# Kernel optimization log

Measured on AMD Instinct MI355X. Metric: run time of the kernel, lower is better.

## Reference

```python
import jax, jax.numpy as jnp
import numpy as np

D_MODEL = 64


def setup_inputs() -> dict:
    key = jax.random.key(0)
    kq, kk, kv, km = jax.random.split(key, 4)
    B, S, d = 8, 4096, D_MODEL
    Q = jax.random.normal(kq, (B, S, d), dtype=jnp.float32)
    K = jax.random.normal(kk, (B, S, d), dtype=jnp.float32)
    V = jax.random.normal(kv, (B, S, d), dtype=jnp.float32)
    mask = jax.random.uniform(km, (S, S), dtype=jnp.float32)
    return {"Q": Q, "K": K, "V": V, "mask": mask}


def reference(Q, K, V, mask):
    scale = 1.0 / np.sqrt(D_MODEL).astype(np.float32)
    # scores: [B, S, S]
    scores = jnp.einsum("bqd,bkd->bqk", Q, K) * scale
    probs = jax.nn.softmax(scores, axis=-1)
    # post-softmax multiplicative mask + renormalization over masked probs
    masked = probs * mask[None, :, :]
    masked = masked / jnp.sum(masked, axis=-1, keepdims=True)
    return jnp.einsum("bqk,bkd->bqd", masked, V)
```

## Files before the change

### kernel.cpp

```cpp
#include <hip/hip_runtime.h>
#include <hip/hip_bf16.h>

#define S_LEN 4096
#define DMODEL 64
#define QBLK 128
#define NQT (S_LEN / QBLK)
#define KBLK 32
#define NKT (S_LEN / KBLK)
#define NSPLIT 4
#define NROWS ((size_t)8 * S_LEN)
#define NELEM ((size_t)8 * S_LEN * DMODEL)
#define TSZ 2048
#define QSCALE 0.180336880f

typedef __attribute__((ext_vector_type(8))) short bf16x8;
typedef __attribute__((ext_vector_type(4))) float f32x4;
typedef __attribute__((ext_vector_type(8))) unsigned short us8;
typedef __attribute__((ext_vector_type(4))) unsigned int u32x4;

#define LDS_BARRIER()                                            \
    do {                                                         \
        asm volatile("s_waitcnt lgkmcnt(0)" ::: "memory");       \
        __builtin_amdgcn_s_barrier();                            \
    } while (0)

__device__ __forceinline__ float bf2f(unsigned short u) {
    unsigned int x = ((unsigned int)u) << 16;
    return __builtin_bit_cast(float, x);
}
__device__ __forceinline__ unsigned short f2bf(float f) {
    unsigned int u = __builtin_bit_cast(unsigned int, f);
    u += 0x7FFFu + ((u >> 16) & 1u);
    return (unsigned short)(u >> 16);
}
__device__ __forceinline__ unsigned int packbf2(float lo, float hi) {
    __hip_bfloat162 h = __float22bfloat162_rn(float2{lo, hi});
    unsigned int w;
    __builtin_memcpy(&w, &h, sizeof(w));
    return w;
}
__device__ __forceinline__ bf16x8 cvt8s(const float* __restrict__ p, float c) {
    f32x4 a = *(const f32x4*)p;
    f32x4 b = *(const f32x4*)(p + 4);
    bf16x8 r;
    r[0] = (short)f2bf(a[0] * c); r[1] = (short)f2bf(a[1] * c);
    r[2] = (short)f2bf(a[2] * c); r[3] = (short)f2bf(a[3] * c);
    r[4] = (short)f2bf(b[0] * c); r[5] = (short)f2bf(b[1] * c);
    r[6] = (short)f2bf(b[2] * c); r[7] = (short)f2bf(b[3] * c);
    return r;
}

__global__ __launch_bounds__(256)
void convert_all(const float* __restrict__ K, const float* __restrict__ V,
                 const float* __restrict__ M,
                 unsigned short* __restrict__ Ktt, unsigned short* __restrict__ Vtt,
                 unsigned short* __restrict__ Mt) {
    const int t = threadIdx.x;
    int bid = blockIdx.x;

    if (bid < 1024) {
        const int b  = bid >> 7;
        const int kt = bid & 127;
        const int l = t & 63, frag = t >> 6;
        const int j = l & 15, g = l >> 4;
        const int row = kt * KBLK + ((frag >> 1) & 1) * 16 + j;
        const int col = (frag & 1) * 32 + g * 8;
        const float* src = K + ((size_t)b * S_LEN + row) * DMODEL + col;
        f32x4 a = *(const f32x4*)src;
        f32x4 c = *(const f32x4*)(src + 4);
        us8 o;
        o[0] = f2bf(a[0]); o[1] = f2bf(a[1]); o[2] = f2bf(a[2]); o[3] = f2bf(a[3]);
        o[4] = f2bf(c[0]); o[5] = f2bf(c[1]); o[6] = f2bf(c[2]); o[7] = f2bf(c[3]);
        *(us8*)(Ktt + ((size_t)(b * NKT + kt)) * TSZ + t * 8) = o;
    } else if (bid < 2048) {
        bid -= 1024;
        __shared__ unsigned short lk[KBLK][68];
        const int b  = bid >> 7;
        const int kt = bid & 127;
        {
            const int key = t >> 3, d0 = (t & 7) * 8;
            const float* src = V + ((size_t)b * S_LEN + kt * KBLK + key) * DMODEL + d0;
            f32x4 a = *(const f32x4*)src;
            f32x4 c = *(const f32x4*)(src + 4);
            lk[key][d0 + 0] = f2bf(a[0]); lk[key][d0 + 1] = f2bf(a[1]);
            lk[key][d0 + 2] = f2bf(a[2]); lk[key][d0 + 3] = f2bf(a[3]);
            lk[key][d0 + 4] = f2bf(c[0]); lk[key][d0 + 5] = f2bf(c[1]);
            lk[key][d0 + 6] = f2bf(c[2]); lk[key][d0 + 7] = f2bf(c[3]);
        }
        __syncthreads();
        {
            const int l = t & 63, dt = t >> 6;
            const int j = l & 15, g = l >> 4;
            us8 o;
            #pragma unroll
            for (int e = 0; e < 8; ++e) {
                const int key = 16 * (e >> 2) + 4 * g + (e & 3);
                o[e] = lk[key][dt * 16 + j];
            }
            *(us8*)(Vtt + ((size_t)(b * NKT + kt)) * TSZ + t * 8) = o;
        }
    } else {
        bid -= 2048;
        const int qt  = bid >> 8;
        const int rem = bid & 255;
        const int kt  = rem >> 1;
        const int h   = rem & 1;
        const int l = t & 63, w = t >> 6;
        const int j = l & 15, g = l >> 4;
        const int row = qt * QBLK + w * 32 + h * 16 + j;
        const float* src = M + ((size_t)row) * S_LEN + kt * KBLK;
        f32x4 a = *(const f32x4*)(src + 4 * g);
        f32x4 c = *(const f32x4*)(src + 16 + 4 * g);
        us8 o;
        o[0] = f2bf(a[0]); o[1] = f2bf(a[1]); o[2] = f2bf(a[2]); o[3] = f2bf(a[3]);
        o[4] = f2bf(c[0]); o[5] = f2bf(c[1]); o[6] = f2bf(c[2]); o[7] = f2bf(c[3]);
        *(us8*)(Mt + (((size_t)(qt * NKT + kt)) * 2 + h) * TSZ + t * 8) = o;
    }
}

template <int SPLITS>
__global__ __launch_bounds__(256, 4)
void attn_frag(const float* __restrict__ Q,
               const unsigned short* __restrict__ Ktt,
               const unsigned short* __restrict__ Vtt,
               const unsigned short* __restrict__ Mt,
               float* __restrict__ Pacc, float* __restrict__ Plsum,
               float* __restrict__ O) {
    __shared__ __align__(16) unsigned short S[16384];

    const int t    = threadIdx.x;
    const int wave = t >> 6;
    const int l    = t & 63;
    const int g    = l >> 4;
    const int j    = l & 15;

    const int bid = blockIdx.x;
    const int b   = bid & 7;
    const int qt  = (bid >> 3) & 31;
    const int sp  = (SPLITS > 1) ? (bid >> 8) : 0;
    const int nsteps = NKT / SPLITS;
    const int qrowA = qt * QBLK + wave * 32 + j;
    const int qrowB = qrowA + 16;
    const size_t rowA = (size_t)b * S_LEN + qrowA;
    const size_t rowB = rowA + 16;

    const float* Qb = Q + (size_t)b * S_LEN * DMODEL;
    const bf16x8 qf0a = cvt8s(Qb + (size_t)qrowA * DMODEL + g * 8, QSCALE);
    const bf16x8 qf1a = cvt8s(Qb + (size_t)qrowA * DMODEL + g * 8 + 32, QSCALE);
    const bf16x8 qf0b = cvt8s(Qb + (size_t)qrowB * DMODEL + g * 8, QSCALE);
    const bf16x8 qf1b = cvt8s(Qb + (size_t)qrowB * DMODEL + g * 8 + 32, QSCALE);

    bf16x8 vones;
    #pragma unroll
    for (int e = 0; e < 8; ++e) vones[e] = (short)0x3F80;

    f32x4 accA[4], accB[4];
    #pragma unroll
    for (int dt = 0; dt < 4; ++dt) {
        accA[dt] = f32x4{0.f, 0.f, 0.f, 0.f};
        accB[dt] = f32x4{0.f, 0.f, 0.f, 0.f};
    }
    f32x4 acclA = {0.f, 0.f, 0.f, 0.f};
    f32x4 acclB = {0.f, 0.f, 0.f, 0.f};

    const int kt0 = sp * nsteps;
    const unsigned short* pk = Ktt + (size_t)(b * NKT + kt0) * TSZ + t * 8;
    const unsigned short* pv = Vtt + (size_t)(b * NKT + kt0) * TSZ + t * 8;
    const unsigned short* pm = Mt + ((size_t)(qt * NKT + kt0) * 2) * TSZ + t * 8;

    auto compute_tile = [&](int bi, us8 m0, us8 m1) {
        bf16x8 kf0 = *(const bf16x8*)&S[bi * 2048 + 0 * 512 + l * 8];
        bf16x8 kf1 = *(const bf16x8*)&S[bi * 2048 + 1 * 512 + l * 8];
        bf16x8 kf2 = *(const bf16x8*)&S[bi * 2048 + 2 * 512 + l * 8];
        bf16x8 kf3 = *(const bf16x8*)&S[bi * 2048 + 3 * 512 + l * 8];

        f32x4 sA0 = {0.f, 0.f, 0.f, 0.f}, sA1 = {0.f, 0.f, 0.f, 0.f};
        f32x4 sB0 = {0.f, 0.f, 0.f, 0.f}, sB1 = {0.f, 0.f, 0.f, 0.f};
        sA0 = __builtin_amdgcn_mfma_f32_16x16x32_bf16(kf0, qf0a, sA0, 0, 0, 0);
        sB0 = __builtin_amdgcn_mfma_f32_16x16x32_bf16(kf0, qf0b, sB0, 0, 0, 0);
        sA0 = __builtin_amdgcn_mfma_f32_16x16x32_bf16(kf1, qf1a, sA0, 0, 0, 0);
        sB0 = __builtin_amdgcn_mfma_f32_16x16x32_bf16(kf1, qf1b, sB0, 0, 0, 0);
        sA1 = __builtin_amdgcn_mfma_f32_16x16x32_bf16(kf2, qf0a, sA1, 0, 0, 0);
        sB1 = __builtin_amdgcn_mfma_f32_16x16x32_bf16(kf2, qf0b, sB1, 0, 0, 0);
        sA1 = __builtin_amdgcn_mfma_f32_16x16x32_bf16(kf3, qf1a, sA1, 0, 0, 0);
        sB1 = __builtin_amdgcn_mfma_f32_16x16x32_bf16(kf3, qf1b, sB1, 0, 0, 0);

        float eA0[4], eA1[4], eB0[4], eB1[4];
        #pragma unroll
        for (int r = 0; r < 4; ++r) {
            eA0[r] = __builtin_amdgcn_exp2f(sA0[r]) * bf2f(m0[r]);
            eA1[r] = __builtin_amdgcn_exp2f(sA1[r]) * bf2f(m0[4 + r]);
            eB0[r] = __builtin_amdgcn_exp2f(sB0[r]) * bf2f(m1[r]);
            eB1[r] = __builtin_amdgcn_exp2f(sB1[r]) * bf2f(m1[4 + r]);
        }
        u32x4 pwA, pwB;
        pwA[0] = packbf2(eA0[0], eA0[1]); pwA[1] = packbf2(eA0[2], eA0[3]);
        pwA[2] = packbf2(eA1[0], eA1[1]); pwA[3] = packbf2(eA1[2], eA1[3]);
        pwB[0] = packbf2(eB0[0], eB0[1]); pwB[1] = packbf2(eB0[2], eB0[3]);
        pwB[2] = packbf2(eB1[0], eB1[1]); pwB[3] = packbf2(eB1[2], eB1[3]);
        const bf16x8 pfA = __builtin_bit_cast(bf16x8, pwA);
        const bf16x8 pfB = __builtin_bit_cast(bf16x8, pwB);

        acclA = __builtin_amdgcn_mfma_f32_16x16x32_bf16(vones, pfA, acclA, 0, 0, 0);
        acclB = __builtin_amdgcn_mfma_f32_16x16x32_bf16(vones, pfB, acclB, 0, 0, 0);
        #pragma unroll
        for (int dt = 0; dt < 4; ++dt) {
            bf16x8 vf = *(const bf16x8*)&S[8192 + bi * 2048 + dt * 512 + l * 8];
            accA[dt] = __builtin_amdgcn_mfma_f32_16x16x32_bf16(vf, pfA, accA[dt], 0, 0, 0);
            accB[dt] = __builtin_amdgcn_mfma_f32_16x16x32_bf16(vf, pfB, accB[dt], 0, 0, 0);
        }
    };

    {
        us8 a0 = *(const us8*)pk;
        us8 a1 = *(const us8*)(pk + TSZ);
        us8 b0 = *(const us8*)pv;
        us8 b1 = *(const us8*)(pv + TSZ);
        *(us8*)&S[0 * 2048 + t * 8] = a0;
        *(us8*)&S[1 * 2048 + t * 8] = a1;
        *(us8*)&S[8192 + 0 * 2048 + t * 8] = b0;
        *(us8*)&S[8192 + 1 * 2048 + t * 8] = b1;
    }
    us8 kreg0 = *(const us8*)(pk + 2 * TSZ);
    us8 kreg1 = *(const us8*)(pk + 3 * TSZ);
    us8 vreg0 = *(const us8*)(pv + 2 * TSZ);
    us8 vreg1 = *(const us8*)(pv + 3 * TSZ);
    pk += 4 * TSZ; pv += 4 * TSZ;
    LDS_BARRIER();

    for (int P = 0; P < nsteps / 4; ++P) {
        #pragma unroll
        for (int h = 0; h < 2; ++h) {
            const int bw = h ? 0 : 2;
            const int br = h ? 2 : 0;

            *(us8*)&S[bw * 2048 + t * 8]            = kreg0;
            *(us8*)&S[(bw + 1) * 2048 + t * 8]      = kreg1;
            *(us8*)&S[8192 + bw * 2048 + t * 8]     = vreg0;
            *(us8*)&S[8192 + (bw + 1) * 2048 + t * 8] = vreg1;

            kreg0 = *(const us8*)pk; kreg1 = *(const us8*)(pk + TSZ); pk += 2 * TSZ;
            vreg0 = *(const us8*)pv; vreg1 = *(const us8*)(pv + TSZ); pv += 2 * TSZ;

            us8 m00 = *(const us8*)pm;
            us8 m01 = *(const us8*)(pm + TSZ);
            us8 m10 = *(const us8*)(pm + 2 * TSZ);
            us8 m11 = *(const us8*)(pm + 3 * TSZ);
            pm += 4 * TSZ;

            compute_tile(br, m00, m01);
            compute_tile(br + 1, m10, m11);

            LDS_BARRIER();
        }
    }

    const float lsumA = acclA[0];
    const float lsumB = acclB[0];

    if (SPLITS > 1) {
        if (g == 0) {
            Plsum[(size_t)sp * NROWS + rowA] = lsumA;
            Plsum[(size_t)sp * NROWS + rowB] = lsumB;
        }
        float* prA = Pacc + ((size_t)sp * NROWS + rowA) * DMODEL;
        float* prB = Pacc + ((size_t)sp * NROWS + rowB) * DMODEL;
        #pragma unroll
        for (int dt = 0; dt < 4; ++dt) {
            *(f32x4*)(prA + dt * 16 + g * 4) = accA[dt];
            *(f32x4*)(prB + dt * 16 + g * 4) = accB[dt];
        }
    } else {
        const float invA = 1.0f / lsumA;
        const float invB = 1.0f / lsumB;
        float* orA = O + rowA * DMODEL;
        float* orB = O + rowB * DMODEL;
        #pragma unroll
        for (int dt = 0; dt < 4; ++dt) {
            f32x4 oa, ob;
            #pragma unroll
            for (int r = 0; r < 4; ++r) { oa[r] = accA[dt][r] * invA; ob[r] = accB[dt][r] * invB; }
            *(f32x4*)(orA + dt * 16 + g * 4) = oa;
            *(f32x4*)(orB + dt * 16 + g * 4) = ob;
        }
    }
}

template <int SPLITS>
__global__ __launch_bounds__(256)
void reduce_split(const float* __restrict__ Pacc, const float* __restrict__ Plsum,
                  float* __restrict__ O) {
    const int t = threadIdx.x;
    const size_t rid = (size_t)blockIdx.x * 16 + (t >> 4);
    const int seg = (t & 15) * 4;

    float ls = 0.f;
    f32x4 a = {0.f, 0.f, 0.f, 0.f};
    #pragma unroll
    for (int s = 0; s < SPLITS; ++s) {
        ls += Plsum[(size_t)s * NROWS + rid];
        f32x4 v = *(const f32x4*)(Pacc + ((size_t)s * NROWS + rid) * DMODEL + seg);
        a[0] += v[0]; a[1] += v[1]; a[2] += v[2]; a[3] += v[3];
    }
    const float inv = 1.0f / ls;
    f32x4 o = {a[0] * inv, a[1] * inv, a[2] * inv, a[3] * inv};
    *(f32x4*)(O + rid * DMODEL + seg) = o;
}

__global__ __launch_bounds__(256)
void attn_fb(const float* __restrict__ Q, const float* __restrict__ Kf,
             const float* __restrict__ Vf, const float* __restrict__ M,
             float* __restrict__ O) {
    const int t    = threadIdx.x;
    const int wave = t >> 6;
    const int lane = t & 63;
    const int g    = lane >> 4;
    const int j    = lane & 15;
    const int bid  = blockIdx.x;
    const int b    = bid & 7;
    const int qt   = bid >> 3;
    const int qrow = qt * 64 + wave * 16 + j;

    const float* Qb = Q + (size_t)b * S_LEN * DMODEL;
    const bf16x8 qf0 = cvt8s(Qb + (size_t)qrow * DMODEL + g * 8, QSCALE);
    const bf16x8 qf1 = cvt8s(Qb + (size_t)qrow * DMODEL + g * 8 + 32, QSCALE);

    f32x4 acc[4];
    #pragma unroll
    for (int dt = 0; dt < 4; ++dt) acc[dt] = f32x4{0.f, 0.f, 0.f, 0.f};
    float lsum = 0.f;

    const float* Kfb = Kf + (size_t)b * S_LEN * DMODEL;
    const float* Vfb = Vf + (size_t)b * S_LEN * DMODEL;
    const float* mrow = M + (size_t)qrow * S_LEN;

    int kg[8];
    #pragma unroll
    for (int e = 0; e < 8; ++e) kg[e] = 16 * (e >> 2) + 4 * g + (e & 3);

    for (int kt = 0; kt < NKT; ++kt) {
        const int kb = kt * KBLK;
        bf16x8 kf00 = cvt8s(Kfb + (size_t)(kb + j) * DMODEL + g * 8, 1.0f);
        bf16x8 kf01 = cvt8s(Kfb + (size_t)(kb + j) * DMODEL + g * 8 + 32, 1.0f);
        bf16x8 kf10 = cvt8s(Kfb + (size_t)(kb + 16 + j) * DMODEL + g * 8, 1.0f);
        bf16x8 kf11 = cvt8s(Kfb + (size_t)(kb + 16 + j) * DMODEL + g * 8 + 32, 1.0f);

        f32x4 st0 = {0.f, 0.f, 0.f, 0.f};
        f32x4 st1 = {0.f, 0.f, 0.f, 0.f};
        st0 = __builtin_amdgcn_mfma_f32_16x16x32_bf16(kf00, qf0, st0, 0, 0, 0);
        st0 = __builtin_amdgcn_mfma_f32_16x16x32_bf16(kf01, qf1, st0, 0, 0, 0);
        st1 = __builtin_amdgcn_mfma_f32_16x16x32_bf16(kf10, qf0, st1, 0, 0, 0);
        st1 = __builtin_amdgcn_mfma_f32_16x16x32_bf16(kf11, qf1, st1, 0, 0, 0);

        f32x4 m0 = *(const f32x4*)(mrow + kb + g * 4);
        f32x4 m1 = *(const f32x4*)(mrow + kb + 16 + g * 4);

        bf16x8 pf;
        #pragma unroll
        for (int r = 0; r < 4; ++r) {
            float w0 = __builtin_amdgcn_exp2f(st0[r]) * m0[r];
            float w1 = __builtin_amdgcn_exp2f(st1[r]) * m1[r];
            lsum += w0 + w1;
            pf[r]     = (short)f2bf(w0);
            pf[4 + r] = (short)f2bf(w1);
        }

        #pragma unroll
        for (int dt = 0; dt < 4; ++dt) {
            bf16x8 vf;
            #pragma unroll
            for (int e = 0; e < 8; ++e)
                vf[e] = (short)f2bf(Vfb[(size_t)(kb + kg[e]) * DMODEL + dt * 16 + j]);
            acc[dt] = __builtin_amdgcn_mfma_f32_16x16x32_bf16(vf, pf, acc[dt], 0, 0, 0);
        }
    }

    lsum += __shfl_xor(lsum, 16, 64);
    lsum += __shfl_xor(lsum, 32, 64);
    const float inv = 1.0f / lsum;

    float* orow = O + ((size_t)b * S_LEN + qrow) * DMODEL;
    #pragma unroll
    for (int dt = 0; dt < 4; ++dt) {
        f32x4 o;
        #pragma unroll
        for (int r = 0; r < 4; ++r) o[r] = acc[dt][r] * inv;
        *(f32x4*)(orow + dt * 16 + g * 4) = o;
    }
}

extern "C" void kernel_launch(void* const* d_in, const int* in_sizes, int n_in,
                              void* d_out, int out_size, void* d_ws, size_t ws_size,
                              hipStream_t stream) {
    const float* Q = (const float*)d_in[0];
    const float* K = (const float*)d_in[1];
    const float* V = (const float*)d_in[2];
    const float* M = (const float*)d_in[3];
    float* O = (float*)d_out;

    const size_t bytes_kv = 2 * NELEM * 2;
    const size_t bytes_m  = (size_t)S_LEN * S_LEN * 2;

    unsigned short* Ktt = (unsigned short*)d_ws;
    unsigned short* Vtt = Ktt + NELEM;
    unsigned short* Mt  = Vtt + NELEM;

    const size_t need4 = bytes_kv + bytes_m + (size_t)NSPLIT * NROWS * 4
                       + (size_t)NSPLIT * NROWS * DMODEL * 4;

    if (ws_size >= need4) {
        float* Plsum = (float*)((char*)d_ws + bytes_kv + bytes_m);
        float* Pacc  = Plsum + (size_t)NSPLIT * NROWS;
        convert_all<<<10240, 256, 0, stream>>>(K, V, M, Ktt, Vtt, Mt);
        attn_frag<NSPLIT><<<8 * NQT * NSPLIT, 256, 0, stream>>>(
            Q, Ktt, Vtt, Mt, Pacc, Plsum, O);
        reduce_split<NSPLIT><<<(int)(NROWS / 16), 256, 0, stream>>>(Pacc, Plsum, O);
    } else {
        attn_fb<<<512, 256, 0, stream>>>(Q, K, V, M, O);
    }
}
```

Baseline: 94.80 us.

## Load K/V fragments directly from global memory instead of staging through LDS

Removes the shared-memory double buffer and barriers in the attention kernel. Each wave now reads its K and V MFMA fragments straight from global (L2/L1-cached) memory per key tile, with a 2x unrolled loop. This drops the LDS writes, LDS reads and block-wide barriers. In exchange each of the four waves re-reads the same K/V tile from global memory, which raises cache traffic and exposes global latency with less explicit prefetching.

After: 97.74 us. +3.1%, slower.

```diff
diff --git a/kernel.cpp b/kernel.cpp
--- a/kernel.cpp
+++ b/kernel.cpp
@@ -17,12 +17,6 @@
 typedef __attribute__((ext_vector_type(4))) float f32x4;
 typedef __attribute__((ext_vector_type(8))) unsigned short us8;
 typedef __attribute__((ext_vector_type(4))) unsigned int u32x4;
-
-#define LDS_BARRIER()                                            \
-    do {                                                         \
-        asm volatile("s_waitcnt lgkmcnt(0)" ::: "memory");       \
-        __builtin_amdgcn_s_barrier();                            \
-    } while (0)
 
 __device__ __forceinline__ float bf2f(unsigned short u) {
     unsigned int x = ((unsigned int)u) << 16;
@@ -120,14 +114,12 @@
 
 template <int SPLITS>
 __global__ __launch_bounds__(256, 4)
-void attn_frag(const float* __restrict__ Q,
-               const unsigned short* __restrict__ Ktt,
-               const unsigned short* __restrict__ Vtt,
-               const unsigned short* __restrict__ Mt,
-               float* __restrict__ Pacc, float* __restrict__ Plsum,
-               float* __restrict__ O) {
-    __shared__ __align__(16) unsigned short S[16384];
-
+void attn_direct(const float* __restrict__ Q,
+                 const unsigned short* __restrict__ Ktt,
+                 const unsigned short* __restrict__ Vtt,
+                 const unsigned short* __restrict__ Mt,
+                 float* __restrict__ Pacc, float* __restrict__ Plsum,
+                 float* __restrict__ O) {
     const int t    = threadIdx.x;
     const int wave = t >> 6;
     const int l    = t & 63;
@@ -164,15 +156,23 @@
     f32x4 acclB = {0.f, 0.f, 0.f, 0.f};
 
     const int kt0 = sp * nsteps;
-    const unsigned short* pk = Ktt + (size_t)(b * NKT + kt0) * TSZ + t * 8;
-    const unsigned short* pv = Vtt + (size_t)(b * NKT + kt0) * TSZ + t * 8;
+    const unsigned short* pk = Ktt + (size_t)(b * NKT + kt0) * TSZ + l * 8;
+    const unsigned short* pv = Vtt + (size_t)(b * NKT + kt0) * TSZ + l * 8;
     const unsigned short* pm = Mt + ((size_t)(qt * NKT + kt0) * 2) * TSZ + t * 8;
 
-    auto compute_tile = [&](int bi, us8 m0, us8 m1) {
-        bf16x8 kf0 = *(const bf16x8*)&S[bi * 2048 + 0 * 512 + l * 8];
-        bf16x8 kf1 = *(const bf16x8*)&S[bi * 2048 + 1 * 512 + l * 8];
-        bf16x8 kf2 = *(const bf16x8*)&S[bi * 2048 + 2 * 512 + l * 8];
-        bf16x8 kf3 = *(const bf16x8*)&S[bi * 2048 + 3 * 512 + l * 8];
+    #pragma unroll 2
+    for (int s = 0; s < nsteps; ++s) {
+        bf16x8 kf0 = *(const bf16x8*)(pk);
+        bf16x8 kf1 = *(const bf16x8*)(pk + 512);
+        bf16x8 kf2 = *(const bf16x8*)(pk + 1024);
+        bf16x8 kf3 = *(const bf16x8*)(pk + 1536);
+        bf16x8 vf0 = *(const bf16x8*)(pv);
+        bf16x8 vf1 = *(const bf16x8*)(pv + 512);
+        bf16x8 vf2 = *(const bf16x8*)(pv + 1024);
+        bf16x8 vf3 = *(const bf16x8*)(pv + 1536);
+        us8 m0 = *(const us8*)(pm);
+        us8 m1 = *(const us8*)(pm + TSZ);
+        pk += TSZ; pv += TSZ; pm += 2 * TSZ;
 
         f32x4 sA0 = {0.f, 0.f, 0.f, 0.f}, sA1 = {0.f, 0.f, 0.f, 0.f};
         f32x4 sB0 = {0.f, 0.f, 0.f, 0.f}, sB1 = {0.f, 0.f, 0.f, 0.f};
@@ -203,56 +203,14 @@
 
         acclA = __builtin_amdgcn_mfma_f32_16x16x32_bf16(vones, pfA, acclA, 0, 0, 0);
         acclB = __builtin_amdgcn_mfma_f32_16x16x32_bf16(vones, pfB, acclB, 0, 0, 0);
-        #pragma unroll
-        for (int dt = 0; dt < 4; ++dt) {
-            bf16x8 vf = *(const bf16x8*)&S[8192 + bi * 2048 + dt * 512 + l * 8];
-            accA[dt] = __builtin_amdgcn_mfma_f32_16x16x32_bf16(vf, pfA, accA[dt], 0, 0, 0);
-            accB[dt] = __builtin_amdgcn_mfma_f32_16x16x32_bf16(vf, pfB, accB[dt], 0, 0, 0);
-        }
-    };
-
-    {
-        us8 a0 = *(const us8*)pk;
-        us8 a1 = *(const us8*)(pk + TSZ);
-        us8 b0 = *(const us8*)pv;
-        us8 b1 = *(const us8*)(pv + TSZ);
-        *(us8*)&S[0 * 2048 + t * 8] = a0;
-        *(us8*)&S[1 * 2048 + t * 8] = a1;
-        *(us8*)&S[8192 + 0 * 2048 + t * 8] = b0;
-        *(us8*)&S[8192 + 1 * 2048 + t * 8] = b1;
-    }
-    us8 kreg0 = *(const us8*)(pk + 2 * TSZ);
-    us8 kreg1 = *(const us8*)(pk + 3 * TSZ);
-    us8 vreg0 = *(const us8*)(pv + 2 * TSZ);
-    us8 vreg1 = *(const us8*)(pv + 3 * TSZ);
-    pk += 4 * TSZ; pv += 4 * TSZ;
-    LDS_BARRIER();
-
-    for (int P = 0; P < nsteps / 4; ++P) {
-        #pragma unroll
-        for (int h = 0; h < 2; ++h) {
-            const int bw = h ? 0 : 2;
-            const int br = h ? 2 : 0;
-
-            *(us8*)&S[bw * 2048 + t * 8]            = kreg0;
-            *(us8*)&S[(bw + 1) * 2048 + t * 8]      = kreg1;
-            *(us8*)&S[8192 + bw * 2048 + t * 8]     = vreg0;
-            *(us8*)&S[8192 + (bw + 1) * 2048 + t * 8] = vreg1;
-
-            kreg0 = *(const us8*)pk; kreg1 = *(const us8*)(pk + TSZ); pk += 2 * TSZ;
-            vreg0 = *(const us8*)pv; vreg1 = *(const us8*)(pv + TSZ); pv += 2 * TSZ;
-
-            us8 m00 = *(const us8*)pm;
-            us8 m01 = *(const us8*)(pm + TSZ);
-            us8 m10 = *(const us8*)(pm + 2 * TSZ);
-            us8 m11 = *(const us8*)(pm + 3 * TSZ);
-            pm += 4 * TSZ;
-
-            compute_tile(br, m00, m01);
-            compute_tile(br + 1, m10, m11);
-
-            LDS_BARRIER();
-        }
+        accA[0] = __builtin_amdgcn_mfma_f32_16x16x32_bf16(vf0, pfA, accA[0], 0, 0, 0);
+        accB[0] = __builtin_amdgcn_mfma_f32_16x16x32_bf16(vf0, pfB, accB[0], 0, 0, 0);
+        accA[1] = __builtin_amdgcn_mfma_f32_16x16x32_bf16(vf1, pfA, accA[1], 0, 0, 0);
+        accB[1] = __builtin_amdgcn_mfma_f32_16x16x32_bf16(vf1, pfB, accB[1], 0, 0, 0);
+        accA[2] = __builtin_amdgcn_mfma_f32_16x16x32_bf16(vf2, pfA, accA[2], 0, 0, 0);
+        accB[2] = __builtin_amdgcn_mfma_f32_16x16x32_bf16(vf2, pfB, accB[2], 0, 0, 0);
+        accA[3] = __builtin_amdgcn_mfma_f32_16x16x32_bf16(vf3, pfA, accA[3], 0, 0, 0);
+        accB[3] = __builtin_amdgcn_mfma_f32_16x16x32_bf16(vf3, pfB, accB[3], 0, 0, 0);
     }
 
     const float lsumA = acclA[0];
@@ -412,7 +370,7 @@
         float* Plsum = (float*)((char*)d_ws + bytes_kv + bytes_m);
         float* Pacc  = Plsum + (size_t)NSPLIT * NROWS;
         convert_all<<<10240, 256, 0, stream>>>(K, V, M, Ktt, Vtt, Mt);
-        attn_frag<NSPLIT><<<8 * NQT * NSPLIT, 256, 0, stream>>>(
+        attn_direct<NSPLIT><<<8 * NQT * NSPLIT, 256, 0, stream>>>(
             Q, Ktt, Vtt, Mt, Pacc, Plsum, O);
         reduce_split<NSPLIT><<<(int)(NROWS / 16), 256, 0, stream>>>(Pacc, Plsum, O);
     } else {
```
